# Kernel optimization log

Hardware: AMD Instinct MI355X
Metric: run time of the kernel (lower is better)

The kernel has to match this reference:

```python
import jax, jax.numpy as jnp
import numpy as np

B, S, DIN, DOUT = 2, 2048, 4096, 4096


def setup_inputs() -> dict:
    key = jax.random.key(0)
    k1, k2, k3, k4, k5 = jax.random.split(key, 5)
    x = jax.random.normal(k1, (B, S, DIN), dtype=jnp.float32)
    # int8-range weights stored as int32 (faithful to q_int_weight.float() upcast)
    q_int_weight = jax.random.randint(k2, (DIN, DOUT), 0, 256, dtype=jnp.int32)
    scale = jax.random.uniform(k3, (1,), dtype=jnp.float32) * 0.01 + 0.001
    zero_point = jax.random.uniform(k4, (1,), dtype=jnp.float32) * 128.0
    bias = jax.random.normal(k5, (DOUT,), dtype=jnp.float32)
    return {"x": x, "q_int_weight": q_int_weight, "scale": scale,
            "zero_point": zero_point, "bias": bias}


def reference(x, q_int_weight, scale, zero_point, bias):
    # Dequantize: (q - zero_point) * scale, per-tensor affine. Stored [in, out].
    w = (q_int_weight.astype(jnp.float32) - zero_point) * scale  # [DIN, DOUT]
    # F.linear(x_flat, w.t(), bias) == x @ w + bias
    y = jnp.einsum('bsi,io->bso', x, w) + bias  # [B, S, DOUT]
    return y
```

## Files before the change

### kernel.cpp

```cpp
#include <hip/hip_runtime.h>
#include <cstdint>
#include <cstddef>

#define M_DIM 4096
#define N_DIM 4096
#define K_DIM 4096
#define BM 256
#define BN 256
#define BKB 128
#define KTILES (K_DIM / BKB)

typedef __attribute__((ext_vector_type(4))) int i32x4;

__device__ __forceinline__ void async_copy16(const void* g, void* l) {
  __builtin_amdgcn_global_load_lds(
      (const __attribute__((address_space(1))) void*)g,
      (__attribute__((address_space(3))) void*)l,
      16, 0, 0);
}

__global__ __launch_bounds__(256) void convert_x_kernel(
    const float* __restrict__ x, signed char* __restrict__ xi,
    float* __restrict__ sx, float* __restrict__ rs) {
  __shared__ float red[8];
  const int t = threadIdx.x;
  const size_t row = blockIdx.x;
  const float* xr = x + row * (size_t)K_DIM;

  float4 v[4];
  float amax = 0.f;
#pragma unroll
  for (int i = 0; i < 4; ++i) {
    v[i] = *(const float4*)(xr + (i * 256 + t) * 4);
    amax = fmaxf(amax, fmaxf(fmaxf(fabsf(v[i].x), fabsf(v[i].y)),
                             fmaxf(fabsf(v[i].z), fabsf(v[i].w))));
  }
#pragma unroll
  for (int o = 32; o > 0; o >>= 1)
    amax = fmaxf(amax, __shfl_down(amax, o, 64));
  if ((t & 63) == 0) red[t >> 6] = amax;
  __syncthreads();
  amax = fmaxf(fmaxf(fmaxf(red[0], red[1]), fmaxf(red[2], red[3])), 1e-20f);
  const float inv = 127.f / amax;

  int ssum = 0;
  signed char* out = xi + row * (size_t)K_DIM;
#pragma unroll
  for (int i = 0; i < 4; ++i) {
    const int ia = __float2int_rn(v[i].x * inv);
    const int ib = __float2int_rn(v[i].y * inv);
    const int ic = __float2int_rn(v[i].z * inv);
    const int id = __float2int_rn(v[i].w * inv);
    ssum += ia + ib + ic + id;
    const int pk =
        (ia & 255) | ((ib & 255) << 8) | ((ic & 255) << 16) | (id << 24);
    *(int*)(out + (i * 256 + t) * 4) = pk;
  }
  float fs = (float)ssum;
#pragma unroll
  for (int o = 32; o > 0; o >>= 1) fs += __shfl_down(fs, o, 64);
  if ((t & 63) == 0) red[4 + (t >> 6)] = fs;
  __syncthreads();
  if (t == 0) {
    rs[row] = red[4] + red[5] + red[6] + red[7];
    sx[row] = amax * (1.f / 127.f);
  }
}

__global__ __launch_bounds__(256) void convert_w_kernel(
    const int* __restrict__ q, signed char* __restrict__ qsT) {
  __shared__ __align__(16) int qtile[64][68];
  const int t = threadIdx.x;
  const int k0 = (blockIdx.x & 63) << 6;
  const int n0 = (blockIdx.x >> 6) << 6;

  {
    const int c = t & 15;
    const int r0 = t >> 4;
#pragma unroll
    for (int i = 0; i < 4; ++i) {
      const int r = r0 + i * 16;
      const int4 v = *(const int4*)(q + (size_t)(k0 + r) * N_DIM + n0 + c * 4);
      *(int4*)&qtile[r][c * 4] = v;
    }
  }
  __syncthreads();
  {
    const int kc = t & 15;
    const int g = t >> 4;
    int4 v[4];
#pragma unroll
    for (int i = 0; i < 4; ++i) v[i] = *(const int4*)&qtile[kc * 4 + i][g * 4];
#pragma unroll
    for (int j = 0; j < 4; ++j) {
      const int b0 = ((&v[0].x)[j] - 128) & 255;
      const int b1 = ((&v[1].x)[j] - 128) & 255;
      const int b2 = ((&v[2].x)[j] - 128) & 255;
      const int b3 = ((&v[3].x)[j] - 128) & 255;
      const int pk = b0 | (b1 << 8) | (b2 << 16) | (b3 << 24);
      *(int*)(qsT + (size_t)(n0 + g * 4 + j) * K_DIM + k0 + kc * 4) = pk;
    }
  }
}

__global__ __launch_bounds__(512, 2) void gemm_kernel(
    const signed char* __restrict__ A,
    const signed char* __restrict__ Bt,
    const float* __restrict__ bias, const float* __restrict__ sx,
    const float* __restrict__ rs, const float* __restrict__ scale_p,
    const float* __restrict__ zp_p, float* __restrict__ C) {
  __shared__ __align__(16) signed char As[2][BM * BKB];
  __shared__ __align__(16) signed char Bs[2][BN * BKB];

  const int tid = threadIdx.x;
  const int wave = tid >> 6;
  const int lane = tid & 63;
  const int wm = wave >> 2;
  const int wn = wave & 3;

  const int swz = (blockIdx.x & 7) * 32 + (blockIdx.x >> 3);
  const int bm = swz & 15;
  const int bn = swz >> 4;
  const size_t m0 = (size_t)bm * BM;
  const size_t n0 = (size_t)bn * BN;

  const int srow = lane >> 3;
  const int schunk = (lane & 7) ^ srow;

  const int quad = lane >> 4;
  const int lrow = lane & 15;
  const int rsw = lrow & 7;

  const signed char* Abase = A + m0 * K_DIM + schunk * 16;
  const signed char* Bbase = Bt + n0 * K_DIM + schunk * 16;

  i32x4 acc[8][4];
  const i32x4 zero = {0, 0, 0, 0};
#pragma unroll
  for (int i = 0; i < 8; ++i)
#pragma unroll
    for (int j = 0; j < 4; ++j) acc[i][j] = zero;

  auto stage = [&](int b, int k0) {
#pragma unroll
    for (int j = 0; j < 4; ++j) {
      const int rbase = j * 64 + wave * 8;
      const size_t go = (size_t)(rbase + srow) * K_DIM + k0;
      async_copy16(Abase + go, (void*)&As[b][rbase * BKB]);
      async_copy16(Bbase + go, (void*)&Bs[b][rbase * BKB]);
    }
  };

#define LDA(ig)                                                              \
  do {                                                                       \
    _Pragma("unroll") for (int kh = 0; kh < 2; ++kh)                         \
        _Pragma("unroll") for (int t = 0; t < 4; ++t) {                      \
      const int ar = wm * 128 + (ig) * 64 + t * 16 + lrow;                   \
      av[kh][t] =                                                            \
          *(const i32x4*)(as + ar * BKB + ((((kh << 2) | quad) ^ rsw) << 4));\
    }                                                                        \
  } while (0)

#define LDB(jg)                                                              \
  do {                                                                       \
    _Pragma("unroll") for (int kh = 0; kh < 2; ++kh)                         \
        _Pragma("unroll") for (int t = 0; t < 2; ++t) {                      \
      const int br = wn * 64 + ((jg) * 2 + t) * 16 + lrow;                   \
      bv[kh][(jg) * 2 + t] =                                                 \
          *(const i32x4*)(bs + br * BKB + ((((kh << 2) | quad) ^ rsw) << 4));\
    }                                                                        \
  } while (0)

#define MFMA16(ibase, j0)                                                    \
  do {                                                                       \
    __builtin_amdgcn_s_setprio(1);                                           \
    _Pragma("unroll") for (int kh = 0; kh < 2; ++kh)                         \
        _Pragma("unroll") for (int t = 0; t < 4; ++t)                        \
            _Pragma("unroll") for (int j = 0; j < 2; ++j)                    \
        acc[(ibase) + t][(j0) + j] = __builtin_amdgcn_mfma_i32_16x16x64_i8(  \
            av[kh][t], bv[kh][(j0) + j], acc[(ibase) + t][(j0) + j], 0, 0,   \
            0);                                                              \
    __builtin_amdgcn_s_setprio(0);                                           \
  } while (0)

  stage(0, 0);
  asm volatile("s_waitcnt vmcnt(0)" ::: "memory");
  __builtin_amdgcn_s_barrier();

#pragma unroll 2
  for (int kt = 0; kt < KTILES; ++kt) {
    const int buf = kt & 1;
    const signed char* as = As[buf];
    const signed char* bs = Bs[buf];

    if (kt + 1 < KTILES) stage(buf ^ 1, (kt + 1) * BKB);

    i32x4 av[2][4], bv[2][4];

    LDA(0);
    LDB(0);
    __builtin_amdgcn_s_barrier();
    MFMA16(0, 0);
    __builtin_amdgcn_s_barrier();

    LDB(1);
    __builtin_amdgcn_s_barrier();
    MFMA16(0, 2);
    __builtin_amdgcn_s_barrier();

    LDA(1);
    __builtin_amdgcn_s_barrier();
    MFMA16(4, 2);
    __builtin_amdgcn_s_barrier();

    MFMA16(4, 0);

    __builtin_amdgcn_sched_barrier(0);
    asm volatile("s_waitcnt lgkmcnt(0)" ::: "memory");
    asm volatile("s_waitcnt vmcnt(0)" ::: "memory");
    __builtin_amdgcn_sched_barrier(0);
    __builtin_amdgcn_s_barrier();
  }

#undef LDA
#undef LDB
#undef MFMA16

  const float scale = scale_p[0];
  const float c1 = 128.f - zp_p[0];
#pragma unroll
  for (int i = 0; i < 8; ++i) {
    const size_t mbase = m0 + wm * 128 + i * 16 + quad * 4;
    float am[4], bmv[4];
#pragma unroll
    for (int r = 0; r < 4; ++r) {
      const float a = scale * sx[mbase + r];
      am[r] = a;
      bmv[r] = a * c1 * rs[mbase + r];
    }
#pragma unroll
    for (int j = 0; j < 4; ++j) {
      const size_t n = n0 + wn * 64 + j * 16 + lrow;
      const float bv = bias[n];
#pragma unroll
      for (int r = 0; r < 4; ++r) {
        C[(mbase + r) * N_DIM + n] =
            fmaf(am[r], (float)acc[i][j][r], bmv[r] + bv);
      }
    }
  }
}

extern "C" void kernel_launch(void* const* d_in, const int* in_sizes, int n_in,
                              void* d_out, int out_size, void* d_ws,
                              size_t ws_size, hipStream_t stream) {
  const float* x = (const float*)d_in[0];
  const int* q = (const int*)d_in[1];
  const float* scale = (const float*)d_in[2];
  const float* zp = (const float*)d_in[3];
  const float* bias = (const float*)d_in[4];
  float* out = (float*)d_out;

  char* ws = (char*)d_ws;
  signed char* xi = (signed char*)ws;
  signed char* qsT = (signed char*)(ws + ((size_t)16 << 20));
  float* sx = (float*)(ws + ((size_t)32 << 20));
  float* rs = (float*)(ws + ((size_t)32 << 20) + (16 << 10));

  convert_x_kernel<<<4096, 256, 0, stream>>>(x, xi, sx, rs);
  convert_w_kernel<<<4096, 256, 0, stream>>>(q, qsT);
  gemm_kernel<<<256, 512, 0, stream>>>(xi, qsT, bias, sx, rs, scale, zp, out);
}
```

Before: 257.8 us.

## Split tile loads into quarter-stages and interleave with MFMA phases

New measurement: 252.4 us. 2.1% less time.

```diff
diff --git a/kernel.cpp b/kernel.cpp
--- a/kernel.cpp
+++ b/kernel.cpp
@@ -18,6 +18,20 @@
       (__attribute__((address_space(3))) void*)l,
       16, 0, 0);
 }
+
+__device__ __forceinline__ void wait_vm6() {
+  asm volatile("s_waitcnt vmcnt(6)" ::: "memory");
+}
+__device__ __forceinline__ void wait_vm4() {
+  asm volatile("s_waitcnt vmcnt(4)" ::: "memory");
+}
+__device__ __forceinline__ void wait_vm2() {
+  asm volatile("s_waitcnt vmcnt(2)" ::: "memory");
+}
+__device__ __forceinline__ void wait_vm0() {
+  asm volatile("s_waitcnt vmcnt(0)" ::: "memory");
+}
+__device__ __forceinline__ void wait_none() {}
 
 __global__ __launch_bounds__(256) void convert_x_kernel(
     const float* __restrict__ x, signed char* __restrict__ xi,
@@ -141,12 +155,19 @@
 #pragma unroll
     for (int j = 0; j < 4; ++j) acc[i][j] = zero;
 
-  auto stage = [&](int b, int k0) {
-#pragma unroll
-    for (int j = 0; j < 4; ++j) {
-      const int rbase = j * 64 + wave * 8;
+  auto stageA = [&](int b, int k0, int ig) {
+#pragma unroll
+    for (int i = 0; i < 2; ++i) {
+      const int rbase = i * 128 + ig * 64 + wave * 8;
       const size_t go = (size_t)(rbase + srow) * K_DIM + k0;
       async_copy16(Abase + go, (void*)&As[b][rbase * BKB]);
+    }
+  };
+  auto stageB = [&](int b, int k0, int jg) {
+#pragma unroll
+    for (int i = 0; i < 2; ++i) {
+      const int rbase = (i * 2 + (wave >> 2)) * 64 + jg * 32 + (wave & 3) * 8;
+      const size_t go = (size_t)(rbase + srow) * K_DIM + k0;
       async_copy16(Bbase + go, (void*)&Bs[b][rbase * BKB]);
     }
   };
@@ -183,48 +204,65 @@
     __builtin_amdgcn_s_setprio(0);                                           \
   } while (0)
 
-  stage(0, 0);
-  asm volatile("s_waitcnt vmcnt(0)" ::: "memory");
+#define DO_TILE(AS, BS, S0, W0, S1, W1, S2, W2, S3)                          \
+  do {                                                                       \
+    const signed char* as = (AS);                                            \
+    const signed char* bs = (BS);                                            \
+    i32x4 av[2][4], bv[2][4];                                                \
+    LDA(0);                                                                  \
+    LDB(0);                                                                  \
+    S0;                                                                      \
+    W0();                                                                    \
+    __builtin_amdgcn_s_barrier();                                            \
+    MFMA16(0, 0);                                                            \
+    __builtin_amdgcn_s_barrier();                                            \
+    LDB(1);                                                                  \
+    S1;                                                                      \
+    W1();                                                                    \
+    __builtin_amdgcn_s_barrier();                                            \
+    MFMA16(0, 2);                                                            \
+    __builtin_amdgcn_s_barrier();                                            \
+    LDA(1);                                                                  \
+    S2;                                                                      \
+    W2();                                                                    \
+    __builtin_amdgcn_s_barrier();                                            \
+    MFMA16(4, 2);                                                            \
+    __builtin_amdgcn_s_barrier();                                            \
+    S3;                                                                      \
+    MFMA16(4, 0);                                                            \
+  } while (0)
+
+  stageA(0, 0, 0);
+  stageB(0, 0, 0);
+  stageB(0, 0, 1);
+  stageA(0, 0, 1);
+  stageA(1, BKB, 0);
+  stageB(1, BKB, 0);
+  stageB(1, BKB, 1);
+  wait_vm6();
   __builtin_amdgcn_s_barrier();
 
 #pragma unroll 2
-  for (int kt = 0; kt < KTILES; ++kt) {
+  for (int kt = 0; kt < KTILES - 2; ++kt) {
     const int buf = kt & 1;
-    const signed char* as = As[buf];
-    const signed char* bs = Bs[buf];
-
-    if (kt + 1 < KTILES) stage(buf ^ 1, (kt + 1) * BKB);
-
-    i32x4 av[2][4], bv[2][4];
-
-    LDA(0);
-    LDB(0);
-    __builtin_amdgcn_s_barrier();
-    MFMA16(0, 0);
-    __builtin_amdgcn_s_barrier();
-
-    LDB(1);
-    __builtin_amdgcn_s_barrier();
-    MFMA16(0, 2);
-    __builtin_amdgcn_s_barrier();
-
-    LDA(1);
-    __builtin_amdgcn_s_barrier();
-    MFMA16(4, 2);
-    __builtin_amdgcn_s_barrier();
-
-    MFMA16(4, 0);
-
-    __builtin_amdgcn_sched_barrier(0);
-    asm volatile("s_waitcnt lgkmcnt(0)" ::: "memory");
-    asm volatile("s_waitcnt vmcnt(0)" ::: "memory");
-    __builtin_amdgcn_sched_barrier(0);
-    __builtin_amdgcn_s_barrier();
-  }
+    const int k1 = (kt + 1) * BKB;
+    const int k2 = (kt + 2) * BKB;
+    DO_TILE(As[buf], Bs[buf],
+            (stageA(buf ^ 1, k1, 1)), wait_vm6,
+            (stageA(buf, k2, 0)),     wait_vm6,
+            (stageB(buf, k2, 0)),     wait_vm6,
+            (stageB(buf, k2, 1)));
+  }
+
+  DO_TILE(As[0], Bs[0], (stageA(1, 31 * BKB, 1)), wait_vm6, (void)0, wait_vm4,
+          (void)0, wait_vm2, (void)0);
+  DO_TILE(As[1], Bs[1], (void)0, wait_vm0, (void)0, wait_none, (void)0,
+          wait_none, (void)0);
 
 #undef LDA
 #undef LDB
 #undef MFMA16
+#undef DO_TILE
 
   const float scale = scale_p[0];
   const float c1 = 128.f - zp_p[0];
```
